# Kernel tuning notes

Measured on AMD Instinct MI355X. Metric: run time of the kernel, lower is better.

Reference implementation:

```python
import jax, jax.numpy as jnp
import numpy as np

D_K = 64
NEG_INF = -1.0e9


def setup_inputs() -> dict:
    key = jax.random.key(0)
    kq, kk, kv = jax.random.split(key, 3)
    B, H, S, D = 2, 16, 2048, D_K
    Q = jax.random.normal(kq, (B, H, S, D), dtype=jnp.float32)
    K = jax.random.normal(kk, (B, H, S, D), dtype=jnp.float32)
    V = jax.random.normal(kv, (B, H, S, D), dtype=jnp.float32)
    # causal mask: True where attention is DISALLOWED (strict upper triangle)
    attn_mask = jnp.triu(jnp.ones((S, S), dtype=bool), k=1)
    return {"Q": Q, "K": K, "V": V, "attn_mask": attn_mask}


def reference(Q, K, V, attn_mask):
    # scores = Q @ (K / sqrt(d_k))^T  -> [B,H,S,S]
    scale = 1.0 / np.sqrt(D_K).astype(np.float32)
    scores = jnp.einsum("bhqd,bhkd->bhqk", Q, K * scale)
    scores = jnp.where(attn_mask, NEG_INF, scores)  # masked_fill_(mask, -1e9)
    attn = jax.nn.softmax(scores, axis=-1)
    context = jnp.einsum("bhqk,bhkd->bhqd", attn, V)
    return (context, attn)
```

## Files before the change

### kernel.cpp

```cpp
#include <hip/hip_runtime.h>

constexpr int S_LEN = 2048;
constexpr int D_K   = 64;
constexpr int N_BH  = 32;
constexpr int KB    = 64;
constexpr int PLP   = 80;

typedef __attribute__((ext_vector_type(8))) short short8;
typedef __attribute__((ext_vector_type(4))) float f32x4;
typedef unsigned short ushort_t;

__device__ __forceinline__ unsigned short f2bf(float f) {
    unsigned int u = __builtin_bit_cast(unsigned int, f);
    u += 0x7fffu + ((u >> 16) & 1u);
    return (unsigned short)(u >> 16);
}
__device__ __forceinline__ float bf2f(unsigned short h) {
    unsigned int u = ((unsigned int)h) << 16;
    return __builtin_bit_cast(float, u);
}

__global__ __launch_bounds__(256)
void prep_k(const float* __restrict__ K, ushort_t* __restrict__ Kws) {
    const int idx = blockIdx.x * 256 + threadIdx.x;
    const float4* src = (const float4*)K + (size_t)idx * 2;
    float4 a = src[0], b = src[1];
    float x[8] = {a.x, a.y, a.z, a.w, b.x, b.y, b.z, b.w};
    short8 o;
    #pragma unroll
    for (int j = 0; j < 8; ++j) o[j] = (short)f2bf(x[j] * 0.125f);
    *(short8*)(Kws + (size_t)idx * 8) = o;
}

__global__ __launch_bounds__(256)
void prep_v(const float* __restrict__ V, ushort_t* __restrict__ Vws) {
    const int gid = blockIdx.x * 256 + threadIdx.x;
    const int u   = gid & 511;
    const int bc  = gid >> 9;
    const int c   = bc & 31;
    const int bh  = bc >> 5;
    const int kg  = u >> 6;
    const int d   = u & 63;
    const float* vp = V + ((size_t)bh * S_LEN + c * KB + kg * 8) * D_K + d;
    short8 o;
    #pragma unroll
    for (int i = 0; i < 8; ++i) o[i] = (short)f2bf(vp[(size_t)i * D_K]);
    *(short8*)(Vws + ((size_t)(bh * 32 + c) * D_K + d) * KB + kg * 8) = o;
}

__global__ __launch_bounds__(512, 4)
void sdpa_main(const float* __restrict__ Q, const ushort_t* __restrict__ Kws,
               const ushort_t* __restrict__ Vws, float* __restrict__ out)
{
    __shared__ __align__(16) ushort_t Kbuf[2][4096];
    __shared__ __align__(16) ushort_t Vbuf[2][4096];
    __shared__ __align__(16) ushort_t Plds[8][16 * PLP];

    const int tid = threadIdx.x;
    const int w   = tid >> 6;
    const int l   = tid & 63;
    const int lr  = l & 15;
    const int lh  = l >> 4;

    const int b    = blockIdx.x;
    const int s    = b >> 8;
    const int cidx = b & 255;
    const int rmap = cidx & 7;
    const int bh   = cidx >> 3;
    const int qblk = s ? (15 - rmap) : rmap;
    const int q0   = qblk * 128;
    const int qw   = q0 + w * 16;
    const int nch  = 2 * (qblk + 1);

    float* ctx_out  = out;
    float* attn_out = out + (size_t)N_BH * S_LEN * D_K;

    short8 qhi[2], qlo[2];
    {
        const float* qrow = Q + ((size_t)bh * S_LEN + qw + lr) * D_K;
        #pragma unroll
        for (int ds = 0; ds < 2; ++ds) {
            const float4* p4 = (const float4*)(qrow + ds * 32 + lh * 8);
            float4 a = p4[0], bq = p4[1];
            float x[8] = {a.x, a.y, a.z, a.w, bq.x, bq.y, bq.z, bq.w};
            short8 hi, lo;
            #pragma unroll
            for (int j = 0; j < 8; ++j) {
                unsigned short h = f2bf(x[j]);
                hi[j] = (short)h;
                lo[j] = (short)f2bf(x[j] - bf2f(h));
            }
            qhi[ds] = hi; qlo[ds] = lo;
        }
    }

    const short8* Kt  = (const short8*)(Kws + (size_t)bh * S_LEN * D_K);
    const short8* Vt8 = (const short8*)(Vws + (size_t)bh * 32 * 4096);

    const int wrow  = tid >> 3;
    const int wcol  = (tid & 7) << 4;
    const int wphys = wrow * 128 + (wcol ^ ((wrow & 7) << 4));

    const int rsw = (lr & 7) << 4;

    float inv_[4];
    {
        float sum[4] = {0.f, 0.f, 0.f, 0.f};
        short8 kst = Kt[tid];
        *(short8*)((char*)&Kbuf[0][0] + wphys) = kst;
        __syncthreads();
        for (int c = 0; c < nch; ++c) {
            if (c + 1 < nch) kst = Kt[(c + 1) * 512 + tid];
            const char* Kb = (const char*)&Kbuf[c & 1][0];
            #pragma unroll
            for (int nt = 0; nt < 4; ++nt) {
                f32x4 acc = {0.f, 0.f, 0.f, 0.f};
                #pragma unroll
                for (int ks = 0; ks < 2; ++ks) {
                    short8 bk = *(const short8*)(Kb + (nt * 16 + lr) * 128 + ((ks * 64 + lh * 16) ^ rsw));
                    acc = __builtin_amdgcn_mfma_f32_16x16x32_bf16(qhi[ks], bk, acc, 0, 0, 0);
                    acc = __builtin_amdgcn_mfma_f32_16x16x32_bf16(qlo[ks], bk, acc, 0, 0, 0);
                }
                const int kg = c * KB + nt * 16 + lr;
                #pragma unroll
                for (int rr = 0; rr < 4; ++rr) {
                    if (kg <= qw + lh * 4 + rr)
                        sum[rr] += __expf(fminf(acc[rr], 60.f));
                }
            }
            if (c + 1 < nch) *(short8*)((char*)&Kbuf[(c + 1) & 1][0] + wphys) = kst;
            __syncthreads();
        }
        #pragma unroll
        for (int rr = 0; rr < 4; ++rr) {
            float t = sum[rr];
            t += __shfl_xor(t, 1);
            t += __shfl_xor(t, 2);
            t += __shfl_xor(t, 4);
            t += __shfl_xor(t, 8);
            inv_[rr] = 1.f / t;
        }
    }

    f32x4 ctx[4];
    #pragma unroll
    for (int nt = 0; nt < 4; ++nt) ctx[nt] = (f32x4){0.f, 0.f, 0.f, 0.f};

    {
        short8 kst = Kt[tid], vst = Vt8[tid];
        *(short8*)((char*)&Kbuf[0][0] + wphys) = kst;
        *(short8*)((char*)&Vbuf[0][0] + wphys) = vst;
        __syncthreads();
        for (int c = 0; c < nch; ++c) {
            if (c + 1 < nch) {
                kst = Kt[(c + 1) * 512 + tid];
                vst = Vt8[(c + 1) * 512 + tid];
            }
            const char* Kb = (const char*)&Kbuf[c & 1][0];
            const char* Vb = (const char*)&Vbuf[c & 1][0];

            #pragma unroll
            for (int nt = 0; nt < 4; ++nt) {
                f32x4 acc = {0.f, 0.f, 0.f, 0.f};
                #pragma unroll
                for (int ks = 0; ks < 2; ++ks) {
                    short8 bk = *(const short8*)(Kb + (nt * 16 + lr) * 128 + ((ks * 64 + lh * 16) ^ rsw));
                    acc = __builtin_amdgcn_mfma_f32_16x16x32_bf16(qhi[ks], bk, acc, 0, 0, 0);
                    acc = __builtin_amdgcn_mfma_f32_16x16x32_bf16(qlo[ks], bk, acc, 0, 0, 0);
                }
                const int kg = c * KB + nt * 16 + lr;
                #pragma unroll
                for (int rr = 0; rr < 4; ++rr) {
                    const int qg = qw + lh * 4 + rr;
                    float p = (kg <= qg) ? __expf(fminf(acc[rr], 60.f)) * inv_[rr] : 0.f;
                    attn_out[((size_t)bh * S_LEN + qg) * S_LEN + kg] = p;
                    Plds[w][(lh * 4 + rr) * PLP + nt * 16 + lr] = f2bf(p);
                }
            }

            #pragma unroll
            for (int ks = 0; ks < 2; ++ks) {
                short8 pa = *(const short8*)&Plds[w][lr * PLP + ks * 32 + lh * 8];
                #pragma unroll
                for (int nt = 0; nt < 4; ++nt) {
                    short8 vb = *(const short8*)(Vb + (nt * 16 + lr) * 128 + ((ks * 64 + lh * 16) ^ rsw));
                    ctx[nt] = __builtin_amdgcn_mfma_f32_16x16x32_bf16(pa, vb, ctx[nt], 0, 0, 0);
                }
            }

            if (c + 1 < nch) {
                *(short8*)((char*)&Kbuf[(c + 1) & 1][0] + wphys) = kst;
                *(short8*)((char*)&Vbuf[(c + 1) & 1][0] + wphys) = vst;
            }
            __syncthreads();
        }
    }

    #pragma unroll
    for (int nt = 0; nt < 4; ++nt)
        #pragma unroll
        for (int rr = 0; rr < 4; ++rr)
            ctx_out[((size_t)bh * S_LEN + qw + lh * 4 + rr) * D_K + nt * 16 + lr] = ctx[nt][rr];

    const int k0 = nch * KB;
    if (k0 < S_LEN) {
        const float4 z = {0.f, 0.f, 0.f, 0.f};
        for (int rr = 0; rr < 128; ++rr) {
            float* rowp = attn_out + ((size_t)bh * S_LEN + q0 + rr) * S_LEN;
            for (int k = k0 + tid * 4; k < S_LEN; k += 512 * 4)
                *(float4*)(rowp + k) = z;
        }
    }
}

constexpr int LDP = 72;

__global__ __launch_bounds__(256)
void sdpa_fused_v1(const float* __restrict__ Q, const float* __restrict__ K,
                   const float* __restrict__ V, float* __restrict__ out)
{
    __shared__ __align__(16) unsigned short Klds[KB * LDP];
    __shared__ __align__(16) unsigned short Vtlds[D_K * LDP];
    __shared__ __align__(16) unsigned short Pl[4][16 * LDP];

    const int tid = threadIdx.x;
    const int w   = tid >> 6;
    const int l   = tid & 63;
    const int lr  = l & 15;
    const int lh  = l >> 4;

    const int bh   = blockIdx.y;
    const int qblk = (int)gridDim.x - 1 - (int)blockIdx.x;
    const int q0   = qblk * 64;
    const int qw   = q0 + w * 16;
    const int nchunks = qblk + 1;

    const size_t in_base = (size_t)bh * S_LEN * D_K;
    float* ctx_out  = out;
    float* attn_out = out + (size_t)N_BH * S_LEN * D_K;

    short8 qhi[2], qlo[2];
    {
        const float* qrow = Q + in_base + (size_t)(qw + lr) * D_K;
        #pragma unroll
        for (int ds = 0; ds < 2; ++ds) {
            const float4* p4 = (const float4*)(qrow + ds * 32 + lh * 8);
            float4 a = p4[0], b = p4[1];
            float x[8] = {a.x, a.y, a.z, a.w, b.x, b.y, b.z, b.w};
            short8 hi, lo;
            #pragma unroll
            for (int j = 0; j < 8; ++j) {
                unsigned short h = f2bf(x[j]);
                hi[j] = (short)h;
                lo[j] = (short)f2bf(x[j] - bf2f(h));
            }
            qhi[ds] = hi; qlo[ds] = lo;
        }
    }

    const int srow = tid >> 2;
    const int scol = (tid & 3) * 16;
    const float* kstage = K + in_base + (size_t)srow * D_K + scol;
    const float* vstage = V + in_base + (size_t)srow * D_K + scol;

    float inv_[4];
    {
        float sum[4] = {0.f, 0.f, 0.f, 0.f};
        for (int c = 0; c < nchunks; ++c) {
            {
                const float4* kp = (const float4*)(kstage + (size_t)c * KB * D_K);
                float4 a0 = kp[0], a1 = kp[1], a2 = kp[2], a3 = kp[3];
                float x[16] = {a0.x,a0.y,a0.z,a0.w, a1.x,a1.y,a1.z,a1.w,
                               a2.x,a2.y,a2.z,a2.w, a3.x,a3.y,a3.z,a3.w};
                short8 w0, w1;
                #pragma unroll
                for (int j = 0; j < 8; ++j) {
                    w0[j] = (short)f2bf(x[j]     * 0.125f);
                    w1[j] = (short)f2bf(x[j + 8] * 0.125f);
                }
                *(short8*)&Klds[srow * LDP + scol]     = w0;
                *(short8*)&Klds[srow * LDP + scol + 8] = w1;
            }
            __syncthreads();
            #pragma unroll
            for (int nt = 0; nt < 4; ++nt) {
                f32x4 acc = {0.f, 0.f, 0.f, 0.f};
                #pragma unroll
                for (int ks = 0; ks < 2; ++ks) {
                    short8 bk = *(const short8*)&Klds[(nt*16 + lr) * LDP + ks*32 + lh*8];
                    acc = __builtin_amdgcn_mfma_f32_16x16x32_bf16(qhi[ks], bk, acc, 0, 0, 0);
                    acc = __builtin_amdgcn_mfma_f32_16x16x32_bf16(qlo[ks], bk, acc, 0, 0, 0);
                }
                const int kg = c * KB + nt * 16 + lr;
                #pragma unroll
                for (int rr = 0; rr < 4; ++rr) {
                    if (kg <= qw + lh * 4 + rr)
                        sum[rr] += __expf(fminf(acc[rr], 60.f));
                }
            }
            __syncthreads();
        }
        #pragma unroll
        for (int rr = 0; rr < 4; ++rr) {
            float t = sum[rr];
            t += __shfl_xor(t, 1);
            t += __shfl_xor(t, 2);
            t += __shfl_xor(t, 4);
            t += __shfl_xor(t, 8);
            inv_[rr] = 1.f / t;
        }
    }

    f32x4 ctx[4];
    #pragma unroll
    for (int nt = 0; nt < 4; ++nt) ctx[nt] = (f32x4){0.f, 0.f, 0.f, 0.f};

    for (int c = 0; c < nchunks; ++c) {
        {
            const float4* kp = (const float4*)(kstage + (size_t)c * KB * D_K);
            float4 a0 = kp[0], a1 = kp[1], a2 = kp[2], a3 = kp[3];
            float x[16] = {a0.x,a0.y,a0.z,a0.w, a1.x,a1.y,a1.z,a1.w,
                           a2.x,a2.y,a2.z,a2.w, a3.x,a3.y,a3.z,a3.w};
            short8 w0, w1;
            #pragma unroll
            for (int j = 0; j < 8; ++j) {
                w0[j] = (short)f2bf(x[j]     * 0.125f);
                w1[j] = (short)f2bf(x[j + 8] * 0.125f);
            }
            *(short8*)&Klds[srow * LDP + scol]     = w0;
            *(short8*)&Klds[srow * LDP + scol + 8] = w1;

            const float4* vp = (const float4*)(vstage + (size_t)c * KB * D_K);
            float4 b0 = vp[0], b1 = vp[1], b2 = vp[2], b3 = vp[3];
            float y[16] = {b0.x,b0.y,b0.z,b0.w, b1.x,b1.y,b1.z,b1.w,
                           b2.x,b2.y,b2.z,b2.w, b3.x,b3.y,b3.z,b3.w};
            #pragma unroll
            for (int j = 0; j < 16; ++j)
                Vtlds[(scol + j) * LDP + srow] = f2bf(y[j]);
        }
        __syncthreads();

        #pragma unroll
        for (int nt = 0; nt < 4; ++nt) {
            f32x4 acc = {0.f, 0.f, 0.f, 0.f};
            #pragma unroll
            for (int ks = 0; ks < 2; ++ks) {
                short8 bk = *(const short8*)&Klds[(nt*16 + lr) * LDP + ks*32 + lh*8];
                acc = __builtin_amdgcn_mfma_f32_16x16x32_bf16(qhi[ks], bk, acc, 0, 0, 0);
                acc = __builtin_amdgcn_mfma_f32_16x16x32_bf16(qlo[ks], bk, acc, 0, 0, 0);
            }
            const int kg = c * KB + nt * 16 + lr;
            #pragma unroll
            for (int rr = 0; rr < 4; ++rr) {
                const int qg = qw + lh * 4 + rr;
                float p = (kg <= qg) ? __expf(fminf(acc[rr], 60.f)) * inv_[rr] : 0.f;
                attn_out[((size_t)bh * S_LEN + qg) * S_LEN + kg] = p;
                Pl[w][(lh * 4 + rr) * LDP + nt * 16 + lr] = f2bf(p);
            }
        }
        __syncthreads();

        #pragma unroll
        for (int ks = 0; ks < 2; ++ks) {
            short8 pa = *(const short8*)&Pl[w][lr * LDP + ks*32 + lh*8];
            #pragma unroll
            for (int nt = 0; nt < 4; ++nt) {
                short8 vb = *(const short8*)&Vtlds[(nt*16 + lr) * LDP + ks*32 + lh*8];
                ctx[nt] = __builtin_amdgcn_mfma_f32_16x16x32_bf16(pa, vb, ctx[nt], 0, 0, 0);
            }
        }
        __syncthreads();
    }

    #pragma unroll
    for (int nt = 0; nt < 4; ++nt)
        #pragma unroll
        for (int rr = 0; rr < 4; ++rr)
            ctx_out[((size_t)bh * S_LEN + qw + lh * 4 + rr) * D_K + nt * 16 + lr] = ctx[nt][rr];

    const int k0 = nchunks * KB;
    if (k0 < S_LEN) {
        const float4 z = {0.f, 0.f, 0.f, 0.f};
        for (int rr = 0; rr < 64; ++rr) {
            float* rowp = attn_out + ((size_t)bh * S_LEN + q0 + rr) * S_LEN;
            for (int k = k0 + tid * 4; k < S_LEN; k += 256 * 4)
                *(float4*)(rowp + k) = z;
        }
    }
}

extern "C" void kernel_launch(void* const* d_in, const int* in_sizes, int n_in,
                              void* d_out, int out_size, void* d_ws, size_t ws_size,
                              hipStream_t stream)
{
    const float* Q = (const float*)d_in[0];
    const float* K = (const float*)d_in[1];
    const float* V = (const float*)d_in[2];
    float* out = (float*)d_out;

    const size_t ws_needed = (size_t)2 * N_BH * S_LEN * D_K * sizeof(ushort_t);
    if (ws_size >= ws_needed) {
        ushort_t* Kws = (ushort_t*)d_ws;
        ushort_t* Vws = Kws + (size_t)N_BH * S_LEN * D_K;
        prep_k<<<2048, 256, 0, stream>>>(K, Kws);
        prep_v<<<2048, 256, 0, stream>>>(V, Vws);
        sdpa_main<<<512, 512, 0, stream>>>(Q, Kws, Vws, out);
    } else {
        dim3 grid(S_LEN / 64, N_BH);
        sdpa_fused_v1<<<grid, 256, 0, stream>>>(Q, K, V, out);
    }
}
```

Measured before the change: 193.4 us.

## Halve query tile per block, drop low-precision pass-1 MFMA, swizzle P LDS

```diff
diff --git a/kernel.cpp b/kernel.cpp
--- a/kernel.cpp
+++ b/kernel.cpp
@@ -4,7 +4,6 @@
 constexpr int D_K   = 64;
 constexpr int N_BH  = 32;
 constexpr int KB    = 64;
-constexpr int PLP   = 80;
 
 typedef __attribute__((ext_vector_type(8))) short short8;
 typedef __attribute__((ext_vector_type(4))) float f32x4;
@@ -48,13 +47,13 @@
     *(short8*)(Vws + ((size_t)(bh * 32 + c) * D_K + d) * KB + kg * 8) = o;
 }
 
-__global__ __launch_bounds__(512, 4)
+__global__ __launch_bounds__(256, 4)
 void sdpa_main(const float* __restrict__ Q, const ushort_t* __restrict__ Kws,
                const ushort_t* __restrict__ Vws, float* __restrict__ out)
 {
     __shared__ __align__(16) ushort_t Kbuf[2][4096];
     __shared__ __align__(16) ushort_t Vbuf[2][4096];
-    __shared__ __align__(16) ushort_t Plds[8][16 * PLP];
+    __shared__ __align__(16) ushort_t Plds[4][1024];
 
     const int tid = threadIdx.x;
     const int w   = tid >> 6;
@@ -62,22 +61,37 @@
     const int lr  = l & 15;
     const int lh  = l >> 4;
 
-    const int b    = blockIdx.x;
-    const int s    = b >> 8;
-    const int cidx = b & 255;
-    const int rmap = cidx & 7;
-    const int bh   = cidx >> 3;
-    const int qblk = s ? (15 - rmap) : rmap;
-    const int q0   = qblk * 128;
-    const int qw   = q0 + w * 16;
-    const int nch  = 2 * (qblk + 1);
+    const int bx  = blockIdx.x;
+    const int g   = bx >> 8;
+    const int idx = bx & 255;
+    const int bh  = idx >> 3;
+    const int r   = idx & 7;
+    int t;
+    switch (g) {
+        case 0:  t = r;      break;
+        case 1:  t = 15 - r; break;
+        case 2:  t = 16 + r; break;
+        default: t = 31 - r; break;
+    }
+    const int nch = t + 1;
+    const int q0  = t * 64;
+    const int qg_base = q0 + w * 16 + lh * 4;
 
     float* ctx_out  = out;
     float* attn_out = out + (size_t)N_BH * S_LEN * D_K;
 
+    const short8* Kt  = (const short8*)(Kws + (size_t)bh * S_LEN * D_K);
+    const short8* Vt8 = (const short8*)(Vws + (size_t)bh * 32 * 4096);
+
+    const int wrow0  = tid >> 3;
+    const int wcol   = (tid & 7) << 4;
+    const int wphys0 = wrow0 * 128 + (wcol ^ ((wrow0 & 7) << 4));
+    const int wphys1 = wphys0 + 32 * 128;
+    const int rsw    = (lr & 7) << 4;
+
     short8 qhi[2], qlo[2];
     {
-        const float* qrow = Q + ((size_t)bh * S_LEN + qw + lr) * D_K;
+        const float* qrow = Q + ((size_t)bh * S_LEN + q0 + w * 16 + lr) * D_K;
         #pragma unroll
         for (int ds = 0; ds < 2; ++ds) {
             const float4* p4 = (const float4*)(qrow + ds * 32 + lh * 8);
@@ -94,24 +108,66 @@
         }
     }
 
-    const short8* Kt  = (const short8*)(Kws + (size_t)bh * S_LEN * D_K);
-    const short8* Vt8 = (const short8*)(Vws + (size_t)bh * 32 * 4096);
-
-    const int wrow  = tid >> 3;
-    const int wcol  = (tid & 7) << 4;
-    const int wphys = wrow * 128 + (wcol ^ ((wrow & 7) << 4));
-
-    const int rsw = (lr & 7) << 4;
-
     float inv_[4];
     {
         float sum[4] = {0.f, 0.f, 0.f, 0.f};
-        short8 kst = Kt[tid];
-        *(short8*)((char*)&Kbuf[0][0] + wphys) = kst;
+
+        auto p1 = [&](const char* Kb, int c) {
+            #pragma unroll
+            for (int nt = 0; nt < 4; ++nt) {
+                f32x4 acc = {0.f, 0.f, 0.f, 0.f};
+                #pragma unroll
+                for (int ks = 0; ks < 2; ++ks) {
+                    short8 bk = *(const short8*)(Kb + (nt * 16 + lr) * 128 + ((ks * 64 + lh * 16) ^ rsw));
+                    acc = __builtin_amdgcn_mfma_f32_16x16x32_bf16(qhi[ks], bk, acc, 0, 0, 0);
+                }
+                const int kg = c * KB + nt * 16 + lr;
+                #pragma unroll
+                for (int rr = 0; rr < 4; ++rr)
+                    if (kg <= qg_base + rr) sum[rr] += __expf(fminf(acc[rr], 60.f));
+            }
+        };
+
+        short8 kE0 = Kt[tid], kE1 = Kt[tid + 256];
+        *(short8*)((char*)&Kbuf[0][0] + wphys0) = kE0;
+        *(short8*)((char*)&Kbuf[0][0] + wphys1) = kE1;
+        short8 kO0 = Kt[512 + tid], kO1 = Kt[512 + tid + 256];
         __syncthreads();
-        for (int c = 0; c < nch; ++c) {
-            if (c + 1 < nch) kst = Kt[(c + 1) * 512 + tid];
-            const char* Kb = (const char*)&Kbuf[c & 1][0];
+        for (int c = 0; c < nch; c += 2) {
+            if (c + 2 < nch) { kE0 = Kt[(c + 2) * 512 + tid]; kE1 = Kt[(c + 2) * 512 + tid + 256]; }
+            p1((const char*)&Kbuf[0][0], c);
+            if (c + 1 < nch) {
+                *(short8*)((char*)&Kbuf[1][0] + wphys0) = kO0;
+                *(short8*)((char*)&Kbuf[1][0] + wphys1) = kO1;
+            }
+            __syncthreads();
+            if (c + 1 < nch) {
+                if (c + 3 < nch) { kO0 = Kt[(c + 3) * 512 + tid]; kO1 = Kt[(c + 3) * 512 + tid + 256]; }
+                p1((const char*)&Kbuf[1][0], c + 1);
+                if (c + 2 < nch) {
+                    *(short8*)((char*)&Kbuf[0][0] + wphys0) = kE0;
+                    *(short8*)((char*)&Kbuf[0][0] + wphys1) = kE1;
+                }
+                __syncthreads();
+            }
+        }
+        #pragma unroll
+        for (int rr = 0; rr < 4; ++rr) {
+            float s = sum[rr];
+            s += __shfl_xor(s, 1);
+            s += __shfl_xor(s, 2);
+            s += __shfl_xor(s, 4);
+            s += __shfl_xor(s, 8);
+            inv_[rr] = 1.f / s;
+        }
+    }
+
+    f32x4 ctx[4];
+    #pragma unroll
+    for (int nt = 0; nt < 4; ++nt) ctx[nt] = (f32x4){0.f, 0.f, 0.f, 0.f};
+
+    {
+        auto p2 = [&](const char* Kb, const char* Vb, int c) {
             #pragma unroll
             for (int nt = 0; nt < 4; ++nt) {
                 f32x4 acc = {0.f, 0.f, 0.f, 0.f};
@@ -124,75 +180,60 @@
                 const int kg = c * KB + nt * 16 + lr;
                 #pragma unroll
                 for (int rr = 0; rr < 4; ++rr) {
-                    if (kg <= qw + lh * 4 + rr)
-                        sum[rr] += __expf(fminf(acc[rr], 60.f));
-                }
-            }
-            if (c + 1 < nch) *(short8*)((char*)&Kbuf[(c + 1) & 1][0] + wphys) = kst;
-            __syncthreads();
-        }
-        #pragma unroll
-        for (int rr = 0; rr < 4; ++rr) {
-            float t = sum[rr];
-            t += __shfl_xor(t, 1);
-            t += __shfl_xor(t, 2);
-            t += __shfl_xor(t, 4);
-            t += __shfl_xor(t, 8);
-            inv_[rr] = 1.f / t;
-        }
-    }
-
-    f32x4 ctx[4];
-    #pragma unroll
-    for (int nt = 0; nt < 4; ++nt) ctx[nt] = (f32x4){0.f, 0.f, 0.f, 0.f};
-
-    {
-        short8 kst = Kt[tid], vst = Vt8[tid];
-        *(short8*)((char*)&Kbuf[0][0] + wphys) = kst;
-        *(short8*)((char*)&Vbuf[0][0] + wphys) = vst;
-        __syncthreads();
-        for (int c = 0; c < nch; ++c) {
-            if (c + 1 < nch) {
-                kst = Kt[(c + 1) * 512 + tid];
-                vst = Vt8[(c + 1) * 512 + tid];
-            }
-            const char* Kb = (const char*)&Kbuf[c & 1][0];
-            const char* Vb = (const char*)&Vbuf[c & 1][0];
-
-            #pragma unroll
-            for (int nt = 0; nt < 4; ++nt) {
-                f32x4 acc = {0.f, 0.f, 0.f, 0.f};
-                #pragma unroll
-                for (int ks = 0; ks < 2; ++ks) {
-                    short8 bk = *(const short8*)(Kb + (nt * 16 + lr) * 128 + ((ks * 64 + lh * 16) ^ rsw));
-                    acc = __builtin_amdgcn_mfma_f32_16x16x32_bf16(qhi[ks], bk, acc, 0, 0, 0);
-                    acc = __builtin_amdgcn_mfma_f32_16x16x32_bf16(qlo[ks], bk, acc, 0, 0, 0);
-                }
-                const int kg = c * KB + nt * 16 + lr;
-                #pragma unroll
-                for (int rr = 0; rr < 4; ++rr) {
-                    const int qg = qw + lh * 4 + rr;
+                    const int pwr = lh * 4 + rr;
+                    const int qg  = qg_base + rr;
                     float p = (kg <= qg) ? __expf(fminf(acc[rr], 60.f)) * inv_[rr] : 0.f;
                     attn_out[((size_t)bh * S_LEN + qg) * S_LEN + kg] = p;
-                    Plds[w][(lh * 4 + rr) * PLP + nt * 16 + lr] = f2bf(p);
-                }
-            }
-
+                    Plds[w][pwr * 64 + ((nt * 16 + lr) ^ ((pwr & 7) << 3))] = f2bf(p);
+                }
+            }
             #pragma unroll
             for (int ks = 0; ks < 2; ++ks) {
-                short8 pa = *(const short8*)&Plds[w][lr * PLP + ks * 32 + lh * 8];
+                short8 pa = *(const short8*)&Plds[w][lr * 64 + ((ks * 32 + lh * 8) ^ ((lr & 7) << 3))];
                 #pragma unroll
                 for (int nt = 0; nt < 4; ++nt) {
                     short8 vb = *(const short8*)(Vb + (nt * 16 + lr) * 128 + ((ks * 64 + lh * 16) ^ rsw));
                     ctx[nt] = __builtin_amdgcn_mfma_f32_16x16x32_bf16(pa, vb, ctx[nt], 0, 0, 0);
                 }
             }
-
+        };
+
+        short8 kE0 = Kt[tid],        kE1 = Kt[tid + 256];
+        short8 vE0 = Vt8[tid],       vE1 = Vt8[tid + 256];
+        *(short8*)((char*)&Kbuf[0][0] + wphys0) = kE0;
+        *(short8*)((char*)&Kbuf[0][0] + wphys1) = kE1;
+        *(short8*)((char*)&Vbuf[0][0] + wphys0) = vE0;
+        *(short8*)((char*)&Vbuf[0][0] + wphys1) = vE1;
+        short8 kO0 = Kt[512 + tid],  kO1 = Kt[512 + tid + 256];
+        short8 vO0 = Vt8[512 + tid], vO1 = Vt8[512 + tid + 256];
+        __syncthreads();
+        for (int c = 0; c < nch; c += 2) {
+            if (c + 2 < nch) {
+                kE0 = Kt[(c + 2) * 512 + tid];  kE1 = Kt[(c + 2) * 512 + tid + 256];
+                vE0 = Vt8[(c + 2) * 512 + tid]; vE1 = Vt8[(c + 2) * 512 + tid + 256];
+            }
+            p2((const char*)&Kbuf[0][0], (const char*)&Vbuf[0][0], c);
             if (c + 1 < nch) {
-                *(short8*)((char*)&Kbuf[(c + 1) & 1][0] + wphys) = kst;
-                *(short8*)((char*)&Vbuf[(c + 1) & 1][0] + wphys) = vst;
+                *(short8*)((char*)&Kbuf[1][0] + wphys0) = kO0;
+                *(short8*)((char*)&Kbuf[1][0] + wphys1) = kO1;
+                *(short8*)((char*)&Vbuf[1][0] + wphys0) = vO0;
+                *(short8*)((char*)&Vbuf[1][0] + wphys1) = vO1;
             }
             __syncthreads();
+            if (c + 1 < nch) {
+                if (c + 3 < nch) {
+                    kO0 = Kt[(c + 3) * 512 + tid];  kO1 = Kt[(c + 3) * 512 + tid + 256];
+                    vO0 = Vt8[(c + 3) * 512 + tid]; vO1 = Vt8[(c + 3) * 512 + tid + 256];
+                }
+                p2((const char*)&Kbuf[1][0], (const char*)&Vbuf[1][0], c + 1);
+                if (c + 2 < nch) {
+                    *(short8*)((char*)&Kbuf[0][0] + wphys0) = kE0;
+                    *(short8*)((char*)&Kbuf[0][0] + wphys1) = kE1;
+                    *(short8*)((char*)&Vbuf[0][0] + wphys0) = vE0;
+                    *(short8*)((char*)&Vbuf[0][0] + wphys1) = vE1;
+                }
+                __syncthreads();
+            }
         }
     }
 
@@ -200,16 +241,14 @@
     for (int nt = 0; nt < 4; ++nt)
         #pragma unroll
         for (int rr = 0; rr < 4; ++rr)
-            ctx_out[((size_t)bh * S_LEN + qw + lh * 4 + rr) * D_K + nt * 16 + lr] = ctx[nt][rr];
+            ctx_out[((size_t)bh * S_LEN + qg_base + rr) * D_K + nt * 16 + lr] = ctx[nt][rr];
 
     const int k0 = nch * KB;
     if (k0 < S_LEN) {
         const float4 z = {0.f, 0.f, 0.f, 0.f};
-        for (int rr = 0; rr < 128; ++rr) {
-            float* rowp = attn_out + ((size_t)bh * S_LEN + q0 + rr) * S_LEN;
-            for (int k = k0 + tid * 4; k < S_LEN; k += 512 * 4)
-                *(float4*)(rowp + k) = z;
-        }
+        float* rowp = attn_out + ((size_t)bh * S_LEN + q0 + (tid >> 2)) * S_LEN;
+        for (int k = k0 + (tid & 3) * 4; k < S_LEN; k += 16)
+            *(float4*)(rowp + k) = z;
     }
 }
 
@@ -404,7 +443,7 @@
         ushort_t* Vws = Kws + (size_t)N_BH * S_LEN * D_K;
         prep_k<<<2048, 256, 0, stream>>>(K, Kws);
         prep_v<<<2048, 256, 0, stream>>>(V, Vws);
-        sdpa_main<<<512, 512, 0, stream>>>(Q, Kws, Vws, out);
+        sdpa_main<<<1024, 256, 0, stream>>>(Q, Kws, Vws, out);
     } else {
         dim3 grid(S_LEN / 64, N_BH);
         sdpa_fused_v1<<<grid, 256, 0, stream>>>(Q, K, V, out);
```

Result: faster. 173.4 us (-10.3%).
